# Kernel optimization log

Measured on AMD Instinct MI355X. Metric: run time of the kernel, lower is better.

Reference implementation:

```python
import jax, jax.numpy as jnp
import numpy as np


def setup_inputs() -> dict:
    key = jax.random.key(0)
    # [batch, 2 (real/imag), proj_nums, det_nums]
    x = jax.random.normal(key, (16, 2, 1024, 1024), dtype=jnp.float32)
    return {"x": x}


def reference(x) -> jnp.ndarray:
    # Split stacked real/imag channels -> complex frequency-domain sinogram.
    re, im = jnp.split(x, 2, axis=1)          # each [B, 1, P, D]
    c = (re + 1j * im).astype(jnp.complex64)
    # Batched row-wise inverse FFT along detector axis (replaces the
    # per-(batch, row) Python loop of cuFFT calls in the original).
    y = jnp.real(jnp.fft.ifft(jnp.fft.ifftshift(c, axes=-1), axis=-1))
    # Global min-max normalization over the whole tensor.
    y_min = jnp.min(y)
    y_max = jnp.max(y)
    return (y - y_min) / (y_max - y_min)
```

## Files before the change

kernel.cpp:

```cpp
#include <hip/hip_runtime.h>

#define FFT_N 1024
#define NBLK 4096

typedef float float4n __attribute__((ext_vector_type(4)));

__device__ __forceinline__ int br6(int x) { return (int)(__brev((unsigned)x) >> 26); }

__device__ __forceinline__ unsigned int f2key(float f) {
    unsigned int u = __float_as_uint(f);
    return (u & 0x80000000u) ? ~u : (u | 0x80000000u);
}
__device__ __forceinline__ float key2f(unsigned int k) {
    unsigned int u = (k & 0x80000000u) ? (k & 0x7FFFFFFFu) : ~k;
    return __uint_as_float(u);
}

__global__ void init_mm(unsigned int* mm) {
    mm[0] = 0xFFFFFFFFu;
    mm[1] = 0u;
}

__device__ __forceinline__ void dif8(float* Zr, float* Zi) {
    const float R = 0.70710678118654752f;
    float tr, ti;
    tr = Zr[0]-Zr[4]; ti = Zi[0]-Zi[4]; Zr[0]+=Zr[4]; Zi[0]+=Zi[4]; Zr[4]=tr;        Zi[4]=ti;
    tr = Zr[1]-Zr[5]; ti = Zi[1]-Zi[5]; Zr[1]+=Zr[5]; Zi[1]+=Zi[5]; Zr[5]=R*(tr-ti); Zi[5]=R*(tr+ti);
    tr = Zr[2]-Zr[6]; ti = Zi[2]-Zi[6]; Zr[2]+=Zr[6]; Zi[2]+=Zi[6]; Zr[6]=-ti;       Zi[6]=tr;
    tr = Zr[3]-Zr[7]; ti = Zi[3]-Zi[7]; Zr[3]+=Zr[7]; Zi[3]+=Zi[7]; Zr[7]=-R*(tr+ti);Zi[7]=R*(tr-ti);
    tr = Zr[0]-Zr[2]; ti = Zi[0]-Zi[2]; Zr[0]+=Zr[2]; Zi[0]+=Zi[2]; Zr[2]=tr;  Zi[2]=ti;
    tr = Zr[1]-Zr[3]; ti = Zi[1]-Zi[3]; Zr[1]+=Zr[3]; Zi[1]+=Zi[3]; Zr[3]=-ti; Zi[3]=tr;
    tr = Zr[4]-Zr[6]; ti = Zi[4]-Zi[6]; Zr[4]+=Zr[6]; Zi[4]+=Zi[6]; Zr[6]=tr;  Zi[6]=ti;
    tr = Zr[5]-Zr[7]; ti = Zi[5]-Zi[7]; Zr[5]+=Zr[7]; Zi[5]+=Zi[7]; Zr[7]=-ti; Zi[7]=tr;
    tr = Zr[0]-Zr[1]; ti = Zi[0]-Zi[1]; Zr[0]+=Zr[1]; Zi[0]+=Zi[1]; Zr[1]=tr; Zi[1]=ti;
    tr = Zr[2]-Zr[3]; ti = Zi[2]-Zi[3]; Zr[2]+=Zr[3]; Zi[2]+=Zi[3]; Zr[3]=tr; Zi[3]=ti;
    tr = Zr[4]-Zr[5]; ti = Zi[4]-Zi[5]; Zr[4]+=Zr[5]; Zi[4]+=Zi[5]; Zr[5]=tr; Zi[5]=ti;
    tr = Zr[6]-Zr[7]; ti = Zi[6]-Zi[7]; Zr[6]+=Zr[7]; Zi[6]+=Zi[7]; Zr[7]=tr; Zi[7]=ti;
}

template <bool USE_ATOMIC>
__global__ __launch_bounds__(256, 4) void hifft_rows(const float* __restrict__ x,
                                                     float* __restrict__ out,
                                                     float* __restrict__ partials,
                                                     unsigned int* __restrict__ mm) {
    const int t    = threadIdx.x;
    const int lane = t & 63;
    const int wid  = t >> 6;
    const int row  = blockIdx.x * 4 + wid;
    const int b    = row >> 10;
    const int p    = row & 1023;
    const float* re = x + (((size_t)(b * 2)) * 1024 + p) * 1024;
    const float* im = re + (size_t)1024 * 1024;

    float ur[8], ui[8], pr[8], pi[8];
    {
        const float4n* a = (const float4n*)(re + 8 * lane);
        const float4n* bq = (const float4n*)(re + 512 + 8 * lane);
        const float4n* c4 = (const float4n*)(im + 8 * lane);
        const float4n* d4 = (const float4n*)(im + 512 + 8 * lane);
        float4n v0 = a[0], v1 = a[1], w0 = bq[0], w1 = bq[1];
        float4n y0 = c4[0], y1 = c4[1], z0 = d4[0], z1 = d4[1];
        ur[0]=v0.x; ur[1]=v0.y; ur[2]=v0.z; ur[3]=v0.w;
        ur[4]=v1.x; ur[5]=v1.y; ur[6]=v1.z; ur[7]=v1.w;
        pr[0]=w0.x; pr[1]=w0.y; pr[2]=w0.z; pr[3]=w0.w;
        pr[4]=w1.x; pr[5]=w1.y; pr[6]=w1.z; pr[7]=w1.w;
        ui[0]=y0.x; ui[1]=y0.y; ui[2]=y0.z; ui[3]=y0.w;
        ui[4]=y1.x; ui[5]=y1.y; ui[6]=y1.z; ui[7]=y1.w;
        pi[0]=z0.x; pi[1]=z0.y; pi[2]=z0.z; pi[3]=z0.w;
        pi[4]=z1.x; pi[5]=z1.y; pi[6]=z1.z; pi[7]=z1.w;
    }

    float Zr[8], Zi[8];
    {
        const int srcd = (64 - lane) & 63;
        float q_r = __shfl(ur[0], srcd), q_i = __shfl(ui[0], srcd);
        float v_r = __shfl(pr[0], srcd), v_i = __shfl(pi[0], srcd);
        if (lane == 0) { q_r = pr[0]; q_i = pi[0]; v_r = ur[0]; v_i = ui[0]; }
        float s, c;
        __sincosf(6.135923151542565e-3f * (float)(8 * lane), &s, &c);
        float Ar = pr[0] + ur[0] + q_r + v_r;
        float Ai = pi[0] + ui[0] - q_i - v_i;
        float Br = pr[0] - ur[0] + q_r - v_r;
        float Bi = pi[0] - ui[0] - q_i + v_i;
        Zr[0] = Ar - (c * Bi + s * Br);
        Zi[0] = Ai + (c * Br - s * Bi);
    }
    #pragma unroll
    for (int j = 1; j < 8; ++j) {
        float q_r = __shfl_xor(ur[8 - j], 63), q_i = __shfl_xor(ui[8 - j], 63);
        float v_r = __shfl_xor(pr[8 - j], 63), v_i = __shfl_xor(pi[8 - j], 63);
        float s, c;
        __sincosf(6.135923151542565e-3f * (float)(8 * lane + j), &s, &c);
        float Ar = pr[j] + ur[j] + q_r + v_r;
        float Ai = pi[j] + ui[j] - q_i - v_i;
        float Br = pr[j] - ur[j] + q_r - v_r;
        float Bi = pi[j] - ui[j] - q_i + v_i;
        Zr[j] = Ar - (c * Bi + s * Br);
        Zi[j] = Ai + (c * Br - s * Bi);
    }

    #pragma unroll
    for (int st = 0; st < 6; ++st) {
        const int h   = 32 >> st;
        const bool hi = (lane & h) != 0;
        const float sgn = hi ? -1.0f : 1.0f;
        if (h > 1) {
            const int j = lane & (h - 1);
            float ang = hi ? (3.14159265358979323846f / (float)h) * (float)j : 0.0f;
            float ws, wc;
            __sincosf(ang, &ws, &wc);
            #pragma unroll
            for (int r = 0; r < 8; ++r) {
                float prt = __shfl_xor(Zr[r], h);
                float pit = __shfl_xor(Zi[r], h);
                float t1 = fmaf(sgn, Zr[r], prt);
                float t2 = fmaf(sgn, Zi[r], pit);
                Zr[r] = t1 * wc - t2 * ws;
                Zi[r] = t1 * ws + t2 * wc;
            }
        } else {
            #pragma unroll
            for (int r = 0; r < 8; ++r) {
                float prt = __shfl_xor(Zr[r], 1);
                float pit = __shfl_xor(Zi[r], 1);
                Zr[r] = fmaf(sgn, Zr[r], prt);
                Zi[r] = fmaf(sgn, Zi[r], pit);
            }
        }
    }

    const int n1 = br6(lane);
    #pragma unroll
    for (int r = 1; r < 8; ++r) {
        float ang = 1.2271846303085129e-2f * (float)(r * n1);
        float s, c;
        __sincosf(ang, &s, &c);
        float xr = Zr[r], xi = Zi[r];
        Zr[r] = xr * c - xi * s;
        Zi[r] = xr * s + xi * c;
    }

    dif8(Zr, Zi);

    constexpr int BR3_[8] = {0, 4, 2, 6, 1, 5, 3, 7};
    const float SC = 4.8828125e-4f;
    float* orow = out + (size_t)row * FFT_N + 2 * n1;
    float vmin = INFINITY, vmax = -INFINITY;
    #pragma unroll
    for (int r = 0; r < 8; ++r) {
        float a = Zr[r] * SC;
        float bb = Zi[r] * SC;
        vmin = fminf(vmin, fminf(a, bb));
        vmax = fmaxf(vmax, fmaxf(a, bb));
        *reinterpret_cast<float2*>(orow + 128 * BR3_[r]) = make_float2(a, bb);
    }

    #pragma unroll
    for (int off = 32; off >= 1; off >>= 1) {
        vmin = fminf(vmin, __shfl_xor(vmin, off));
        vmax = fmaxf(vmax, __shfl_xor(vmax, off));
    }
    __shared__ float smn[4], smx[4];
    if ((t & 63) == 0) { smn[wid] = vmin; smx[wid] = vmax; }
    __syncthreads();
    if (t == 0) {
        float mn = fminf(fminf(smn[0], smn[1]), fminf(smn[2], smn[3]));
        float mx = fmaxf(fmaxf(smx[0], smx[1]), fmaxf(smx[2], smx[3]));
        if (USE_ATOMIC) {
            atomicMin(&mm[0], f2key(mn));
            atomicMax(&mm[1], f2key(mx));
        } else {
            partials[2 * blockIdx.x]     = mn;
            partials[2 * blockIdx.x + 1] = mx;
        }
    }
}

__global__ __launch_bounds__(256) void normalize_r(float* __restrict__ out,
                                                   const float* __restrict__ partials,
                                                   int n4) {
    float mn = INFINITY, mx = -INFINITY;
    #pragma unroll
    for (int it = 0; it < NBLK / 256; ++it) {
        float2 v = reinterpret_cast<const float2*>(partials)[threadIdx.x + it * 256];
        mn = fminf(mn, v.x);
        mx = fmaxf(mx, v.y);
    }
    #pragma unroll
    for (int off = 32; off >= 1; off >>= 1) {
        mn = fminf(mn, __shfl_xor(mn, off));
        mx = fmaxf(mx, __shfl_xor(mx, off));
    }
    __shared__ float smn[4], smx[4], bmm[2];
    const int wid = threadIdx.x >> 6;
    if ((threadIdx.x & 63) == 0) { smn[wid] = mn; smx[wid] = mx; }
    __syncthreads();
    if (threadIdx.x == 0) {
        bmm[0] = fminf(fminf(smn[0], smn[1]), fminf(smn[2], smn[3]));
        bmm[1] = fmaxf(fmaxf(smx[0], smx[1]), fmaxf(smx[2], smx[3]));
    }
    __syncthreads();
    const float MN  = bmm[0];
    const float INV = 1.0f / (bmm[1] - MN);

    float4n* o4 = reinterpret_cast<float4n*>(out);
    for (int i = blockIdx.x * blockDim.x + threadIdx.x; i < n4;
         i += gridDim.x * blockDim.x) {
        float4n v = o4[i];
        v.x = (v.x - MN) * INV;
        v.y = (v.y - MN) * INV;
        v.z = (v.z - MN) * INV;
        v.w = (v.w - MN) * INV;
        __builtin_nontemporal_store(v, &o4[i]);
    }
}

template <bool FROM_KEYS>
__global__ __launch_bounds__(256) void normalize_k(float* __restrict__ out,
                                                   const void* __restrict__ mmv,
                                                   int n4) {
    float mn, mx;
    if (FROM_KEYS) {
        const unsigned int* mm = (const unsigned int*)mmv;
        mn = key2f(mm[0]); mx = key2f(mm[1]);
    } else {
        const float* mm = (const float*)mmv;
        mn = mm[0]; mx = mm[1];
    }
    const float inv = 1.0f / (mx - mn);
    float4n* o4 = reinterpret_cast<float4n*>(out);
    for (int i = blockIdx.x * blockDim.x + threadIdx.x; i < n4;
         i += gridDim.x * blockDim.x) {
        float4n v = o4[i];
        v.x = (v.x - mn) * inv;
        v.y = (v.y - mn) * inv;
        v.z = (v.z - mn) * inv;
        v.w = (v.w - mn) * inv;
        o4[i] = v;
    }
}

extern "C" void kernel_launch(void* const* d_in, const int* in_sizes, int n_in,
                              void* d_out, int out_size, void* d_ws, size_t ws_size,
                              hipStream_t stream) {
    const float* x = (const float*)d_in[0];
    float* out = (float*)d_out;
    const int n4 = out_size / 4;

    if (ws_size >= (size_t)(2 * NBLK) * sizeof(float)) {
        float* partials = (float*)d_ws;
        hipLaunchKernelGGL((hifft_rows<false>), dim3(NBLK), dim3(256), 0, stream,
                           x, out, partials, nullptr);
        hipLaunchKernelGGL(normalize_r, dim3(2048), dim3(256), 0, stream,
                           out, partials, n4);
    } else {
        unsigned int* mm = (unsigned int*)d_ws;
        hipLaunchKernelGGL(init_mm, dim3(1), dim3(1), 0, stream, mm);
        hipLaunchKernelGGL((hifft_rows<true>), dim3(NBLK), dim3(256), 0, stream,
                           x, out, nullptr, mm);
        hipLaunchKernelGGL((normalize_k<true>), dim3(2048), dim3(256), 0, stream,
                           out, (const void*)mm, n4);
    }
}
```

Baseline: 62.52 us.

## Process four rows per wave and hoist twiddle sincos out of row loop

```diff
diff --git a/kernel.cpp b/kernel.cpp
--- a/kernel.cpp
+++ b/kernel.cpp
@@ -1,7 +1,7 @@
 #include <hip/hip_runtime.h>
 
 #define FFT_N 1024
-#define NBLK 4096
+#define NBLK4 1024
 
 typedef float float4n __attribute__((ext_vector_type(4)));
 
@@ -39,76 +39,98 @@
 }
 
 template <bool USE_ATOMIC>
-__global__ __launch_bounds__(256, 4) void hifft_rows(const float* __restrict__ x,
-                                                     float* __restrict__ out,
-                                                     float* __restrict__ partials,
-                                                     unsigned int* __restrict__ mm) {
+__global__ __launch_bounds__(256, 4) void hifft4(const float* __restrict__ x,
+                                                 float* __restrict__ out,
+                                                 float* __restrict__ partials,
+                                                 unsigned int* __restrict__ mm) {
     const int t    = threadIdx.x;
     const int lane = t & 63;
     const int wid  = t >> 6;
-    const int row  = blockIdx.x * 4 + wid;
-    const int b    = row >> 10;
-    const int p    = row & 1023;
-    const float* re = x + (((size_t)(b * 2)) * 1024 + p) * 1024;
-    const float* im = re + (size_t)1024 * 1024;
-
-    float ur[8], ui[8], pr[8], pi[8];
-    {
-        const float4n* a = (const float4n*)(re + 8 * lane);
-        const float4n* bq = (const float4n*)(re + 512 + 8 * lane);
-        const float4n* c4 = (const float4n*)(im + 8 * lane);
-        const float4n* d4 = (const float4n*)(im + 512 + 8 * lane);
-        float4n v0 = a[0], v1 = a[1], w0 = bq[0], w1 = bq[1];
-        float4n y0 = c4[0], y1 = c4[1], z0 = d4[0], z1 = d4[1];
-        ur[0]=v0.x; ur[1]=v0.y; ur[2]=v0.z; ur[3]=v0.w;
-        ur[4]=v1.x; ur[5]=v1.y; ur[6]=v1.z; ur[7]=v1.w;
-        pr[0]=w0.x; pr[1]=w0.y; pr[2]=w0.z; pr[3]=w0.w;
-        pr[4]=w1.x; pr[5]=w1.y; pr[6]=w1.z; pr[7]=w1.w;
-        ui[0]=y0.x; ui[1]=y0.y; ui[2]=y0.z; ui[3]=y0.w;
-        ui[4]=y1.x; ui[5]=y1.y; ui[6]=y1.z; ui[7]=y1.w;
-        pi[0]=z0.x; pi[1]=z0.y; pi[2]=z0.z; pi[3]=z0.w;
-        pi[4]=z1.x; pi[5]=z1.y; pi[6]=z1.z; pi[7]=z1.w;
-    }
-
-    float Zr[8], Zi[8];
-    {
-        const int srcd = (64 - lane) & 63;
-        float q_r = __shfl(ur[0], srcd), q_i = __shfl(ui[0], srcd);
-        float v_r = __shfl(pr[0], srcd), v_i = __shfl(pi[0], srcd);
-        if (lane == 0) { q_r = pr[0]; q_i = pi[0]; v_r = ur[0]; v_i = ui[0]; }
-        float s, c;
-        __sincosf(6.135923151542565e-3f * (float)(8 * lane), &s, &c);
-        float Ar = pr[0] + ur[0] + q_r + v_r;
-        float Ai = pi[0] + ui[0] - q_i - v_i;
-        float Br = pr[0] - ur[0] + q_r - v_r;
-        float Bi = pi[0] - ui[0] - q_i + v_i;
-        Zr[0] = Ar - (c * Bi + s * Br);
-        Zi[0] = Ai + (c * Br - s * Bi);
-    }
-    #pragma unroll
-    for (int j = 1; j < 8; ++j) {
-        float q_r = __shfl_xor(ur[8 - j], 63), q_i = __shfl_xor(ui[8 - j], 63);
-        float v_r = __shfl_xor(pr[8 - j], 63), v_i = __shfl_xor(pi[8 - j], 63);
-        float s, c;
-        __sincosf(6.135923151542565e-3f * (float)(8 * lane + j), &s, &c);
-        float Ar = pr[j] + ur[j] + q_r + v_r;
-        float Ai = pi[j] + ui[j] - q_i - v_i;
-        float Br = pr[j] - ur[j] + q_r - v_r;
-        float Bi = pi[j] - ui[j] - q_i + v_i;
-        Zr[j] = Ar - (c * Bi + s * Br);
-        Zi[j] = Ai + (c * Br - s * Bi);
-    }
-
-    #pragma unroll
-    for (int st = 0; st < 6; ++st) {
-        const int h   = 32 >> st;
-        const bool hi = (lane & h) != 0;
-        const float sgn = hi ? -1.0f : 1.0f;
-        if (h > 1) {
-            const int j = lane & (h - 1);
-            float ang = hi ? (3.14159265358979323846f / (float)h) * (float)j : 0.0f;
-            float ws, wc;
-            __sincosf(ang, &ws, &wc);
+    const int wave = blockIdx.x * 4 + wid;
+    const int row0 = wave * 4;
+    const int b    = row0 >> 10;
+    const int p0   = row0 & 1023;
+    const float* re0 = x + (((size_t)(b * 2)) * 1024 + p0) * 1024;
+    const float* im0 = re0 + (size_t)1024 * 1024;
+
+    float pks[8], pkc[8];
+    #pragma unroll
+    for (int j = 0; j < 8; ++j)
+        __sincosf(6.135923151542565e-3f * (float)(8 * lane + j), &pks[j], &pkc[j]);
+
+    float stws[5], stwc[5];
+    #pragma unroll
+    for (int st = 0; st < 5; ++st) {
+        const int h = 32 >> st;
+        float ang = (lane & h) ? (3.14159265358979323846f / (float)h) * (float)(lane & (h - 1))
+                               : 0.0f;
+        __sincosf(ang, &stws[st], &stwc[st]);
+    }
+
+    const int n1 = br6(lane);
+    float lts[7], ltc[7];
+    #pragma unroll
+    for (int r = 1; r < 8; ++r)
+        __sincosf(1.2271846303085129e-2f * (float)(r * n1), &lts[r - 1], &ltc[r - 1]);
+
+    const int srcd = (64 - lane) & 63;
+    constexpr int BR3_[8] = {0, 4, 2, 6, 1, 5, 3, 7};
+    const float SC = 4.8828125e-4f;
+
+    float vmin = INFINITY, vmax = -INFINITY;
+
+    #pragma unroll 1
+    for (int rr = 0; rr < 4; ++rr) {
+        const float* re = re0 + rr * 1024;
+        const float* im = im0 + rr * 1024;
+
+        float ur[8], ui[8], pr[8], pi[8];
+        {
+            const float4n* a  = (const float4n*)(re + 8 * lane);
+            const float4n* bq = (const float4n*)(re + 512 + 8 * lane);
+            const float4n* c4 = (const float4n*)(im + 8 * lane);
+            const float4n* d4 = (const float4n*)(im + 512 + 8 * lane);
+            float4n v0 = a[0], v1 = a[1], w0 = bq[0], w1 = bq[1];
+            float4n y0 = c4[0], y1 = c4[1], z0 = d4[0], z1 = d4[1];
+            ur[0]=v0.x; ur[1]=v0.y; ur[2]=v0.z; ur[3]=v0.w;
+            ur[4]=v1.x; ur[5]=v1.y; ur[6]=v1.z; ur[7]=v1.w;
+            pr[0]=w0.x; pr[1]=w0.y; pr[2]=w0.z; pr[3]=w0.w;
+            pr[4]=w1.x; pr[5]=w1.y; pr[6]=w1.z; pr[7]=w1.w;
+            ui[0]=y0.x; ui[1]=y0.y; ui[2]=y0.z; ui[3]=y0.w;
+            ui[4]=y1.x; ui[5]=y1.y; ui[6]=y1.z; ui[7]=y1.w;
+            pi[0]=z0.x; pi[1]=z0.y; pi[2]=z0.z; pi[3]=z0.w;
+            pi[4]=z1.x; pi[5]=z1.y; pi[6]=z1.z; pi[7]=z1.w;
+        }
+
+        float Zr[8], Zi[8];
+        {
+            float q_r = __shfl(ur[0], srcd), q_i = __shfl(ui[0], srcd);
+            float v_r = __shfl(pr[0], srcd), v_i = __shfl(pi[0], srcd);
+            if (lane == 0) { q_r = pr[0]; q_i = pi[0]; v_r = ur[0]; v_i = ui[0]; }
+            float Ar = pr[0] + ur[0] + q_r + v_r;
+            float Ai = pi[0] + ui[0] - q_i - v_i;
+            float Br = pr[0] - ur[0] + q_r - v_r;
+            float Bi = pi[0] - ui[0] - q_i + v_i;
+            Zr[0] = Ar - (pkc[0] * Bi + pks[0] * Br);
+            Zi[0] = Ai + (pkc[0] * Br - pks[0] * Bi);
+        }
+        #pragma unroll
+        for (int j = 1; j < 8; ++j) {
+            float q_r = __shfl_xor(ur[8 - j], 63), q_i = __shfl_xor(ui[8 - j], 63);
+            float v_r = __shfl_xor(pr[8 - j], 63), v_i = __shfl_xor(pi[8 - j], 63);
+            float Ar = pr[j] + ur[j] + q_r + v_r;
+            float Ai = pi[j] + ui[j] - q_i - v_i;
+            float Br = pr[j] - ur[j] + q_r - v_r;
+            float Bi = pi[j] - ui[j] - q_i + v_i;
+            Zr[j] = Ar - (pkc[j] * Bi + pks[j] * Br);
+            Zi[j] = Ai + (pkc[j] * Br - pks[j] * Bi);
+        }
+
+        #pragma unroll
+        for (int st = 0; st < 5; ++st) {
+            const int h = 32 >> st;
+            const float sgn = (lane & h) ? -1.0f : 1.0f;
+            const float ws = stws[st], wc = stwc[st];
             #pragma unroll
             for (int r = 0; r < 8; ++r) {
                 float prt = __shfl_xor(Zr[r], h);
@@ -118,7 +140,9 @@
                 Zr[r] = t1 * wc - t2 * ws;
                 Zi[r] = t1 * ws + t2 * wc;
             }
-        } else {
+        }
+        {
+            const float sgn = (lane & 1) ? -1.0f : 1.0f;
             #pragma unroll
             for (int r = 0; r < 8; ++r) {
                 float prt = __shfl_xor(Zr[r], 1);
@@ -127,32 +151,25 @@
                 Zi[r] = fmaf(sgn, Zi[r], pit);
             }
         }
-    }
-
-    const int n1 = br6(lane);
-    #pragma unroll
-    for (int r = 1; r < 8; ++r) {
-        float ang = 1.2271846303085129e-2f * (float)(r * n1);
-        float s, c;
-        __sincosf(ang, &s, &c);
-        float xr = Zr[r], xi = Zi[r];
-        Zr[r] = xr * c - xi * s;
-        Zi[r] = xr * s + xi * c;
-    }
-
-    dif8(Zr, Zi);
-
-    constexpr int BR3_[8] = {0, 4, 2, 6, 1, 5, 3, 7};
-    const float SC = 4.8828125e-4f;
-    float* orow = out + (size_t)row * FFT_N + 2 * n1;
-    float vmin = INFINITY, vmax = -INFINITY;
-    #pragma unroll
-    for (int r = 0; r < 8; ++r) {
-        float a = Zr[r] * SC;
-        float bb = Zi[r] * SC;
-        vmin = fminf(vmin, fminf(a, bb));
-        vmax = fmaxf(vmax, fmaxf(a, bb));
-        *reinterpret_cast<float2*>(orow + 128 * BR3_[r]) = make_float2(a, bb);
+
+        #pragma unroll
+        for (int r = 1; r < 8; ++r) {
+            float xr = Zr[r], xi = Zi[r];
+            Zr[r] = xr * ltc[r - 1] - xi * lts[r - 1];
+            Zi[r] = xr * lts[r - 1] + xi * ltc[r - 1];
+        }
+
+        dif8(Zr, Zi);
+
+        float* orow = out + (size_t)(row0 + rr) * FFT_N + 2 * n1;
+        #pragma unroll
+        for (int r = 0; r < 8; ++r) {
+            float a  = Zr[r] * SC;
+            float bb = Zi[r] * SC;
+            vmin = fminf(vmin, fminf(a, bb));
+            vmax = fmaxf(vmax, fmaxf(a, bb));
+            *reinterpret_cast<float2*>(orow + 128 * BR3_[r]) = make_float2(a, bb);
+        }
     }
 
     #pragma unroll
@@ -170,8 +187,7 @@
             atomicMin(&mm[0], f2key(mn));
             atomicMax(&mm[1], f2key(mx));
         } else {
-            partials[2 * blockIdx.x]     = mn;
-            partials[2 * blockIdx.x + 1] = mx;
+            reinterpret_cast<float2*>(partials)[blockIdx.x] = make_float2(mn, mx);
         }
     }
 }
@@ -181,7 +197,7 @@
                                                    int n4) {
     float mn = INFINITY, mx = -INFINITY;
     #pragma unroll
-    for (int it = 0; it < NBLK / 256; ++it) {
+    for (int it = 0; it < NBLK4 / 256; ++it) {
         float2 v = reinterpret_cast<const float2*>(partials)[threadIdx.x + it * 256];
         mn = fminf(mn, v.x);
         mx = fmaxf(mx, v.y);
@@ -247,16 +263,16 @@
     float* out = (float*)d_out;
     const int n4 = out_size / 4;
 
-    if (ws_size >= (size_t)(2 * NBLK) * sizeof(float)) {
+    if (ws_size >= (size_t)(2 * NBLK4) * sizeof(float)) {
         float* partials = (float*)d_ws;
-        hipLaunchKernelGGL((hifft_rows<false>), dim3(NBLK), dim3(256), 0, stream,
+        hipLaunchKernelGGL((hifft4<false>), dim3(NBLK4), dim3(256), 0, stream,
                            x, out, partials, nullptr);
         hipLaunchKernelGGL(normalize_r, dim3(2048), dim3(256), 0, stream,
                            out, partials, n4);
     } else {
         unsigned int* mm = (unsigned int*)d_ws;
         hipLaunchKernelGGL(init_mm, dim3(1), dim3(1), 0, stream, mm);
-        hipLaunchKernelGGL((hifft_rows<true>), dim3(NBLK), dim3(256), 0, stream,
+        hipLaunchKernelGGL((hifft4<true>), dim3(NBLK4), dim3(256), 0, stream,
                            x, out, nullptr, mm);
         hipLaunchKernelGGL((normalize_k<true>), dim3(2048), dim3(256), 0, stream,
                            out, (const void*)mm, n4);
```

Result: slower. 97.43 us (+55.8%).
